# Kernel optimization log

Measured on AMD Instinct MI355X. Metric: run time of the kernel, lower is better.

Reference implementation:

```python
import jax, jax.numpy as jnp
import numpy as np

N_NODES = 50000
N_EDGES = 800000
D_IN = 64
D_HID = 64
N_LAYERS = 3
BN_EPS = 1e-5


def setup_inputs() -> dict:
    key = jax.random.key(0)
    ks = jax.random.split(key, 10)
    x = jax.random.normal(ks[0], (N_NODES, D_IN), dtype=jnp.float32)
    edge_index = jax.random.randint(ks[1], (2, N_EDGES), 0, N_NODES, dtype=jnp.int32)
    # Per-layer GCN weights (in==hid==64 so we can stack) and BatchNorm params.
    Ws = jax.random.normal(ks[2], (N_LAYERS, D_HID, D_HID), dtype=jnp.float32) / np.sqrt(D_HID)
    bs = jnp.zeros((N_LAYERS, D_HID), dtype=jnp.float32)
    gammas = jnp.ones((N_LAYERS, D_HID), dtype=jnp.float32)
    betas = jnp.zeros((N_LAYERS, D_HID), dtype=jnp.float32)
    means = jax.random.normal(ks[3], (N_LAYERS, D_HID), dtype=jnp.float32) * 0.1
    variances = jax.random.uniform(ks[4], (N_LAYERS, D_HID), dtype=jnp.float32, minval=0.5, maxval=1.5)
    lin_w = jax.random.normal(ks[5], (D_HID, 1), dtype=jnp.float32) / np.sqrt(D_HID)
    lin_b = jnp.zeros((1,), dtype=jnp.float32)
    return {"x": x, "edge_index": edge_index, "Ws": Ws, "bs": bs,
            "gammas": gammas, "betas": betas, "means": means,
            "variances": variances, "lin_w": lin_w, "lin_b": lin_b}


def _gnn_forward(x, edge_index, Ws, bs, gammas, betas, means, variances, lin_w, lin_b):
    n = x.shape[0]
    # GCNConv: add self loops, symmetric D^{-1/2}(A+I)D^{-1/2} normalization.
    loop = jnp.arange(n, dtype=edge_index.dtype)
    row = jnp.concatenate([edge_index[0], loop])  # source nodes
    col = jnp.concatenate([edge_index[1], loop])  # target nodes
    deg = jax.ops.segment_sum(jnp.ones(row.shape[0], x.dtype), col, num_segments=n)
    dinv = jax.lax.rsqrt(jnp.maximum(deg, 1.0))  # deg >= 1 from self loops
    norm = (dinv[row] * dinv[col])[:, None]  # [E+N, 1]

    h = x
    for i in range(N_LAYERS):
        h = h @ Ws[i]  # transform first (PyG GCNConv order)
        h = jax.ops.segment_sum(h[row] * norm, col, num_segments=n) + bs[i]
        # BatchNorm1d (eval mode: running stats) + ReLU; dropout is identity in eval.
        h = (h - means[i]) * jax.lax.rsqrt(variances[i] + BN_EPS) * gammas[i] + betas[i]
        h = jax.nn.relu(h)
    out = h @ lin_w + lin_b  # [N, 1]
    return out[:, 0]


def reference(x, edge_index, Ws, bs, gammas, betas, means, variances, lin_w, lin_b):
    return _gnn_forward(x, edge_index, Ws, bs, gammas, betas, means, variances, lin_w, lin_b)
```

## Files before the change

kernel.cpp:

```cpp
#include <hip/hip_runtime.h>
#include <hip/hip_bf16.h>


#define BN_EPS 1e-5f
#define CAP 64
#define CHUNK 4096
#define SEGCAP 5120
#define NBINS_MAX 256

__global__ __launch_bounds__(256) void k_bin_pairs(const int* __restrict__ row,
                                                   const int* __restrict__ col,
                                                   int* __restrict__ gfill,
                                                   unsigned int* __restrict__ gpairs,
                                                   int e, int nbins) {
    __shared__ unsigned int pl[CHUNK];
    __shared__ int bcnt[NBINS_MAX];
    __shared__ int bbase[NBINS_MAX];
    int tid = threadIdx.x;
    int base = blockIdx.x * CHUNK;
    for (int b = tid; b < nbins; b += 256) bcnt[b] = 0;
    __syncthreads();
    int nloc = e - base; if (nloc > CHUNK) nloc = CHUNK;
    #pragma unroll
    for (int it = 0; it < CHUNK / 1024; ++it) {
        int le = (it * 256 + tid) * 4;
        if (le + 3 < nloc) {
            int i4 = (base >> 2) + it * 256 + tid;
            int4 r = ((const int4*)row)[i4];
            int4 c = ((const int4*)col)[i4];
            atomicAdd(&bcnt[c.x >> 8], 1); pl[le + 0] = (unsigned)r.x | ((unsigned)c.x << 16);
            atomicAdd(&bcnt[c.y >> 8], 1); pl[le + 1] = (unsigned)r.y | ((unsigned)c.y << 16);
            atomicAdd(&bcnt[c.z >> 8], 1); pl[le + 2] = (unsigned)r.z | ((unsigned)c.z << 16);
            atomicAdd(&bcnt[c.w >> 8], 1); pl[le + 3] = (unsigned)r.w | ((unsigned)c.w << 16);
        } else {
            for (int j = 0; j < 4; ++j) {
                if (le + j < nloc) {
                    int rr = row[base + le + j];
                    int cc = col[base + le + j];
                    atomicAdd(&bcnt[cc >> 8], 1);
                    pl[le + j] = (unsigned)rr | ((unsigned)cc << 16);
                }
            }
        }
    }
    __syncthreads();
    for (int b = tid; b < nbins; b += 256) {
        bbase[b] = atomicAdd(&gfill[b], bcnt[b]);
        bcnt[b] = 0;
    }
    __syncthreads();
    for (int i = tid; i < nloc; i += 256) {
        unsigned int p = pl[i];
        int bin = p >> 24;
        int off = atomicAdd(&bcnt[bin], 1);
        int pos = bbase[bin] + off;
        if (pos < SEGCAP) gpairs[(size_t)bin * SEGCAP + pos] = p;
    }
}

__global__ __launch_bounds__(256) void k_bucket_build(const unsigned int* __restrict__ gpairs,
                                                      const int* __restrict__ gfill,
                                                      int* __restrict__ cnt,
                                                      unsigned short* __restrict__ bucket,
                                                      int n) {
    __shared__ unsigned short lb[256 * CAP];
    __shared__ int lc[256];
    int tid = threadIdx.x;
    int bin = blockIdx.x;
    lc[tid] = 0;
    __syncthreads();
    int m = gfill[bin]; if (m > SEGCAP) m = SEGCAP;
    const unsigned int* seg = gpairs + (size_t)bin * SEGCAP;
    for (int i = tid; i < m; i += 256) {
        unsigned int p = seg[i];
        int src = p & 0xffff;
        int dl = (p >> 16) & 255;
        int pos = atomicAdd(&lc[dl], 1);
        if (pos < CAP) lb[dl * CAP + pos] = (unsigned short)src;
    }
    __syncthreads();
    int nodebase = bin << 8;
    const int4* lb4 = (const int4*)lb;
    int4* gb4 = (int4*)bucket;
    for (int i = tid; i < 256 * 8; i += 256) {
        int rrow = i >> 3;
        int gnode = nodebase + rrow;
        if (gnode < n) gb4[(size_t)gnode * 8 + (i & 7)] = lb4[i];
    }
    int gnode = nodebase + tid;
    if (gnode < n) cnt[gnode] = lc[tid];
}

__global__ __launch_bounds__(256) void k_prescale(const float* __restrict__ x,
                                                  const int* __restrict__ cnt,
                                                  float* __restrict__ t, int n16) {
    int i = blockIdx.x * blockDim.x + threadIdx.x;
    if (i < n16) {
        int node = i >> 4;
        float d = rsqrtf((float)(cnt[node] + 1));
        float4 v = ((const float4*)x)[i];
        v.x *= d; v.y *= d; v.z *= d; v.w *= d;
        ((float4*)t)[i] = v;
    }
}

template<int LAYER, bool FINAL>
__global__ __launch_bounds__(256, 4) void k_layer(const float* __restrict__ t,
                                                  const int* __restrict__ cnt,
                                                  const unsigned short* __restrict__ bucket,
                                                  const float* __restrict__ W,
                                                  const float* __restrict__ bias,
                                                  const float* __restrict__ gamma,
                                                  const float* __restrict__ beta,
                                                  const float* __restrict__ mean,
                                                  const float* __restrict__ var,
                                                  float* __restrict__ hout,
                                                  const float* __restrict__ lw,
                                                  const float* __restrict__ lb,
                                                  float* __restrict__ outp, int n) {
    int lane = threadIdx.x & 63;
    float wreg[64];
    #pragma unroll
    for (int k = 0; k < 64; ++k) wreg[k] = W[k * 64 + lane];
    float bn_b  = bias[lane];
    float bn_m  = mean[lane];
    float bn_s  = gamma[lane] * rsqrtf(var[lane] + BN_EPS);
    float bn_be = beta[lane];
    float lwv   = FINAL ? lw[lane] : 0.f;
    int g = lane >> 4;
    int fl = (lane & 15) << 2;
    int wave = (blockIdx.x * blockDim.x + threadIdx.x) >> 6;
    int nwaves = (gridDim.x * blockDim.x) >> 6;
    for (int node = wave; node < n; node += nwaves) {
        int c = cnt[node];
        int myidx = (int)bucket[node * CAP + lane];
        float4 acc = {0.f, 0.f, 0.f, 0.f};
        int sub = 0;
        for (; sub + 8 <= c; sub += 8) {
            int sA = __shfl(myidx, sub + g, 64);
            int sB = __shfl(myidx, sub + 4 + g, 64);
            float4 vA = *(const float4*)(t + (size_t)sA * 64 + fl);
            float4 vB = *(const float4*)(t + (size_t)sB * 64 + fl);
            acc.x += vA.x; acc.y += vA.y; acc.z += vA.z; acc.w += vA.w;
            acc.x += vB.x; acc.y += vB.y; acc.z += vB.z; acc.w += vB.w;
        }
        for (; sub < c; sub += 4) {
            int j = sub + g;
            int jj = (j < c) ? j : c - 1;
            int sA = __shfl(myidx, jj, 64);
            if (j < c) {
                float4 v = *(const float4*)(t + (size_t)sA * 64 + fl);
                acc.x += v.x; acc.y += v.y; acc.z += v.z; acc.w += v.w;
            }
        }
        acc.x += __shfl_down(acc.x, 32, 64); acc.y += __shfl_down(acc.y, 32, 64);
        acc.z += __shfl_down(acc.z, 32, 64); acc.w += __shfl_down(acc.w, 32, 64);
        acc.x += __shfl_down(acc.x, 16, 64); acc.y += __shfl_down(acc.y, 16, 64);
        acc.z += __shfl_down(acc.z, 16, 64); acc.w += __shfl_down(acc.w, 16, 64);
        if (lane < 16) {
            float4 self = *(const float4*)(t + (size_t)node * 64 + fl);
            acc.x += self.x; acc.y += self.y; acc.z += self.z; acc.w += self.w;
        }
        float y = 0.f;
        #pragma unroll
        for (int q = 0; q < 16; ++q) {
            float ax = __shfl(acc.x, q, 64);
            float ay = __shfl(acc.y, q, 64);
            float az = __shfl(acc.z, q, 64);
            float aw = __shfl(acc.w, q, 64);
            y = fmaf(ax, wreg[4 * q + 0], y);
            y = fmaf(ay, wreg[4 * q + 1], y);
            y = fmaf(az, wreg[4 * q + 2], y);
            y = fmaf(aw, wreg[4 * q + 3], y);
        }
        float di = rsqrtf((float)(c + 1));
        float z = fmaf(y, di, bn_b);
        float h = fmaxf(fmaf(z - bn_m, bn_s, bn_be), 0.f);
        if (FINAL) {
            float p = h * lwv;
            p += __shfl_down(p, 32, 64);
            p += __shfl_down(p, 16, 64);
            p += __shfl_down(p, 8, 64);
            p += __shfl_down(p, 4, 64);
            p += __shfl_down(p, 2, 64);
            p += __shfl_down(p, 1, 64);
            if (lane == 0) outp[node] = p + lb[0];
        } else {
            hout[(size_t)node * 64 + lane] = h * di;
        }
    }
}

extern "C" void kernel_launch(void* const* d_in, const int* in_sizes, int n_in,
                              void* d_out, int out_size, void* d_ws, size_t ws_size,
                              hipStream_t stream) {
    const float* x    = (const float*)d_in[0];
    const int*   ei   = (const int*)d_in[1];
    const float* Ws   = (const float*)d_in[2];
    const float* bs   = (const float*)d_in[3];
    const float* gam  = (const float*)d_in[4];
    const float* bet  = (const float*)d_in[5];
    const float* mean = (const float*)d_in[6];
    const float* var  = (const float*)d_in[7];
    const float* lw   = (const float*)d_in[8];
    const float* lb   = (const float*)d_in[9];
    float* out = (float*)d_out;

    const int n = in_sizes[0] / 64;
    const int e = in_sizes[1] / 2;
    const int* row = ei;
    const int* col = ei + e;
    const int nbins = (n + 255) >> 8;

    int*   ws_i = (int*)d_ws;
    float* ws_f = (float*)d_ws;
    int* cnt = ws_i;
    int* gfill = ws_i + n;
    unsigned short* bucket = (unsigned short*)(ws_i + n + 256);
    float* tbuf = ws_f + n + 256 + 32 * (size_t)n;
    float* hbuf = tbuf + 64 * (size_t)n;
    unsigned int* gpairs = (unsigned int*)tbuf;

    int nb_p1 = (e + CHUNK - 1) / CHUNK;
    int n16 = n * 16;
    int nb_ps = (n16 + 255) / 256;
    int nb_ly = 1024;

    hipMemsetAsync(gfill, 0, 256 * sizeof(int), stream);
    k_bin_pairs<<<nb_p1, 256, 0, stream>>>(row, col, gfill, gpairs, e, nbins);
    k_bucket_build<<<nbins, 256, 0, stream>>>(gpairs, gfill, cnt, bucket, n);
    k_prescale<<<nb_ps, 256, 0, stream>>>(x, cnt, tbuf, n16);

    k_layer<0, false><<<nb_ly, 256, 0, stream>>>(tbuf, cnt, bucket, Ws,
                                                 bs, gam, bet, mean, var,
                                                 hbuf, nullptr, nullptr, nullptr, n);
    k_layer<1, false><<<nb_ly, 256, 0, stream>>>(hbuf, cnt, bucket, Ws + 4096,
                                                 bs + 64, gam + 64, bet + 64, mean + 64, var + 64,
                                                 tbuf, nullptr, nullptr, nullptr, n);
    k_layer<2, true><<<nb_ly, 256, 0, stream>>>(tbuf, cnt, bucket, Ws + 8192,
                                                bs + 128, gam + 128, bet + 128, mean + 128, var + 128,
                                                nullptr, lw, lb, out, n);
}
```

Before: 264.3 us.

## Store gathered node features in fp16 and regroup the per-node gather

The prescaled input and intermediate hidden features are now stored as fp16, which halves the bytes read in the random neighbor gathers of each layer. The gather is regrouped so that 8 lanes each load 8 halves per neighbor, covering 8 neighbors per load across the wave. Tail iterations use masking instead of a separate remainder loop. Occupancy hints and the grid size are also raised. Accumulation stays in fp32, but fp16 storage adds rounding error to the activations across the three layers.

```diff
diff --git a/kernel.cpp b/kernel.cpp
--- a/kernel.cpp
+++ b/kernel.cpp
@@ -1,5 +1,6 @@
 #include <hip/hip_runtime.h>
 #include <hip/hip_bf16.h>
+#include <hip/hip_fp16.h>
 
 
 #define BN_EPS 1e-5f
@@ -93,19 +94,24 @@
 
 __global__ __launch_bounds__(256) void k_prescale(const float* __restrict__ x,
                                                   const int* __restrict__ cnt,
-                                                  float* __restrict__ t, int n16) {
+                                                  __half* __restrict__ t, int n8) {
     int i = blockIdx.x * blockDim.x + threadIdx.x;
-    if (i < n16) {
-        int node = i >> 4;
+    if (i < n8) {
+        int node = i >> 3;
         float d = rsqrtf((float)(cnt[node] + 1));
-        float4 v = ((const float4*)x)[i];
-        v.x *= d; v.y *= d; v.z *= d; v.w *= d;
-        ((float4*)t)[i] = v;
+        const float4* xp = (const float4*)(x + (size_t)i * 8);
+        float4 a = xp[0], b = xp[1];
+        union { __half2 h2[4]; uint4 u; } o;
+        o.h2[0] = __floats2half2_rn(a.x * d, a.y * d);
+        o.h2[1] = __floats2half2_rn(a.z * d, a.w * d);
+        o.h2[2] = __floats2half2_rn(b.x * d, b.y * d);
+        o.h2[3] = __floats2half2_rn(b.z * d, b.w * d);
+        *(uint4*)(t + (size_t)i * 8) = o.u;
     }
 }
 
 template<int LAYER, bool FINAL>
-__global__ __launch_bounds__(256, 4) void k_layer(const float* __restrict__ t,
+__global__ __launch_bounds__(256, 6) void k_layer(const __half* __restrict__ t,
                                                   const int* __restrict__ cnt,
                                                   const unsigned short* __restrict__ bucket,
                                                   const float* __restrict__ W,
@@ -114,7 +120,7 @@
                                                   const float* __restrict__ beta,
                                                   const float* __restrict__ mean,
                                                   const float* __restrict__ var,
-                                                  float* __restrict__ hout,
+                                                  __half* __restrict__ hout,
                                                   const float* __restrict__ lw,
                                                   const float* __restrict__ lb,
                                                   float* __restrict__ outp, int n) {
@@ -127,52 +133,66 @@
     float bn_s  = gamma[lane] * rsqrtf(var[lane] + BN_EPS);
     float bn_be = beta[lane];
     float lwv   = FINAL ? lw[lane] : 0.f;
-    int g = lane >> 4;
-    int fl = (lane & 15) << 2;
+    int g = lane >> 3;
+    int q = lane & 7;
+    int qo = q << 3;
     int wave = (blockIdx.x * blockDim.x + threadIdx.x) >> 6;
     int nwaves = (gridDim.x * blockDim.x) >> 6;
+    union HV { float4 f4; __half2 h2[4]; };
     for (int node = wave; node < n; node += nwaves) {
         int c = cnt[node];
         int myidx = (int)bucket[node * CAP + lane];
-        float4 acc = {0.f, 0.f, 0.f, 0.f};
-        int sub = 0;
-        for (; sub + 8 <= c; sub += 8) {
-            int sA = __shfl(myidx, sub + g, 64);
-            int sB = __shfl(myidx, sub + 4 + g, 64);
-            float4 vA = *(const float4*)(t + (size_t)sA * 64 + fl);
-            float4 vB = *(const float4*)(t + (size_t)sB * 64 + fl);
-            acc.x += vA.x; acc.y += vA.y; acc.z += vA.z; acc.w += vA.w;
-            acc.x += vB.x; acc.y += vB.y; acc.z += vB.z; acc.w += vB.w;
-        }
-        for (; sub < c; sub += 4) {
-            int j = sub + g;
-            int jj = (j < c) ? j : c - 1;
-            int sA = __shfl(myidx, jj, 64);
-            if (j < c) {
-                float4 v = *(const float4*)(t + (size_t)sA * 64 + fl);
-                acc.x += v.x; acc.y += v.y; acc.z += v.z; acc.w += v.w;
-            }
-        }
-        acc.x += __shfl_down(acc.x, 32, 64); acc.y += __shfl_down(acc.y, 32, 64);
-        acc.z += __shfl_down(acc.z, 32, 64); acc.w += __shfl_down(acc.w, 32, 64);
-        acc.x += __shfl_down(acc.x, 16, 64); acc.y += __shfl_down(acc.y, 16, 64);
-        acc.z += __shfl_down(acc.z, 16, 64); acc.w += __shfl_down(acc.w, 16, 64);
-        if (lane < 16) {
-            float4 self = *(const float4*)(t + (size_t)node * 64 + fl);
-            acc.x += self.x; acc.y += self.y; acc.z += self.z; acc.w += self.w;
-        }
-        float y = 0.f;
+        float acc[8] = {0.f, 0.f, 0.f, 0.f, 0.f, 0.f, 0.f, 0.f};
+        for (int sub = 0; sub < c; sub += 16) {
+            int j1 = sub + g;
+            int j2 = sub + 8 + g;
+            int cm1 = c - 1;
+            int i1 = __shfl(myidx, (j1 < cm1 ? j1 : cm1), 64);
+            int i2 = __shfl(myidx, (j2 < cm1 ? j2 : cm1), 64);
+            float m1 = (j1 < c) ? 1.f : 0.f;
+            float m2 = (j2 < c) ? 1.f : 0.f;
+            HV v1, v2;
+            v1.f4 = *(const float4*)(t + ((size_t)i1 << 6) + qo);
+            v2.f4 = *(const float4*)(t + ((size_t)i2 << 6) + qo);
+            #pragma unroll
+            for (int p = 0; p < 4; ++p) {
+                float2 a = __half22float2(v1.h2[p]);
+                float2 b = __half22float2(v2.h2[p]);
+                acc[2 * p]     = fmaf(m1, a.x, acc[2 * p]);
+                acc[2 * p + 1] = fmaf(m1, a.y, acc[2 * p + 1]);
+                acc[2 * p]     = fmaf(m2, b.x, acc[2 * p]);
+                acc[2 * p + 1] = fmaf(m2, b.y, acc[2 * p + 1]);
+            }
+        }
+        {
+            float ms = (g == 0) ? 1.f : 0.f;
+            HV vs;
+            vs.f4 = *(const float4*)(t + ((size_t)node << 6) + qo);
+            #pragma unroll
+            for (int p = 0; p < 4; ++p) {
+                float2 a = __half22float2(vs.h2[p]);
+                acc[2 * p]     = fmaf(ms, a.x, acc[2 * p]);
+                acc[2 * p + 1] = fmaf(ms, a.y, acc[2 * p + 1]);
+            }
+        }
         #pragma unroll
-        for (int q = 0; q < 16; ++q) {
-            float ax = __shfl(acc.x, q, 64);
-            float ay = __shfl(acc.y, q, 64);
-            float az = __shfl(acc.z, q, 64);
-            float aw = __shfl(acc.w, q, 64);
-            y = fmaf(ax, wreg[4 * q + 0], y);
-            y = fmaf(ay, wreg[4 * q + 1], y);
-            y = fmaf(az, wreg[4 * q + 2], y);
-            y = fmaf(aw, wreg[4 * q + 3], y);
-        }
+        for (int i = 0; i < 8; ++i) {
+            acc[i] += __shfl_down(acc[i], 32, 64);
+            acc[i] += __shfl_down(acc[i], 16, 64);
+            acc[i] += __shfl_down(acc[i], 8, 64);
+        }
+        float y0 = 0.f, y1 = 0.f;
+        #pragma unroll
+        for (int q2 = 0; q2 < 8; ++q2) {
+            #pragma unroll
+            for (int i = 0; i < 8; i += 2) {
+                float a0 = __shfl(acc[i], q2, 64);
+                float a1 = __shfl(acc[i + 1], q2, 64);
+                y0 = fmaf(a0, wreg[8 * q2 + i], y0);
+                y1 = fmaf(a1, wreg[8 * q2 + i + 1], y1);
+            }
+        }
+        float y = y0 + y1;
         float di = rsqrtf((float)(c + 1));
         float z = fmaf(y, di, bn_b);
         float h = fmaxf(fmaf(z - bn_m, bn_s, bn_be), 0.f);
@@ -186,7 +206,7 @@
             p += __shfl_down(p, 1, 64);
             if (lane == 0) outp[node] = p + lb[0];
         } else {
-            hout[(size_t)node * 64 + lane] = h * di;
+            hout[(size_t)node * 64 + lane] = __float2half_rn(h * di);
         }
     }
 }
@@ -212,32 +232,31 @@
     const int* col = ei + e;
     const int nbins = (n + 255) >> 8;
 
-    int*   ws_i = (int*)d_ws;
-    float* ws_f = (float*)d_ws;
+    int* ws_i = (int*)d_ws;
     int* cnt = ws_i;
     int* gfill = ws_i + n;
     unsigned short* bucket = (unsigned short*)(ws_i + n + 256);
-    float* tbuf = ws_f + n + 256 + 32 * (size_t)n;
-    float* hbuf = tbuf + 64 * (size_t)n;
-    unsigned int* gpairs = (unsigned int*)tbuf;
+    __half* t16 = (__half*)(ws_i + n + 256 + 32 * (size_t)n);
+    __half* h16 = t16 + 64 * (size_t)n;
+    unsigned int* gpairs = (unsigned int*)t16;
 
     int nb_p1 = (e + CHUNK - 1) / CHUNK;
-    int n16 = n * 16;
-    int nb_ps = (n16 + 255) / 256;
-    int nb_ly = 1024;
+    int n8 = n * 8;
+    int nb_ps = (n8 + 255) / 256;
+    int nb_ly = 1536;
 
     hipMemsetAsync(gfill, 0, 256 * sizeof(int), stream);
     k_bin_pairs<<<nb_p1, 256, 0, stream>>>(row, col, gfill, gpairs, e, nbins);
     k_bucket_build<<<nbins, 256, 0, stream>>>(gpairs, gfill, cnt, bucket, n);
-    k_prescale<<<nb_ps, 256, 0, stream>>>(x, cnt, tbuf, n16);
-
-    k_layer<0, false><<<nb_ly, 256, 0, stream>>>(tbuf, cnt, bucket, Ws,
+    k_prescale<<<nb_ps, 256, 0, stream>>>(x, cnt, t16, n8);
+
+    k_layer<0, false><<<nb_ly, 256, 0, stream>>>(t16, cnt, bucket, Ws,
                                                  bs, gam, bet, mean, var,
-                                                 hbuf, nullptr, nullptr, nullptr, n);
-    k_layer<1, false><<<nb_ly, 256, 0, stream>>>(hbuf, cnt, bucket, Ws + 4096,
+                                                 h16, nullptr, nullptr, nullptr, n);
+    k_layer<1, false><<<nb_ly, 256, 0, stream>>>(h16, cnt, bucket, Ws + 4096,
                                                  bs + 64, gam + 64, bet + 64, mean + 64, var + 64,
-                                                 tbuf, nullptr, nullptr, nullptr, n);
-    k_layer<2, true><<<nb_ly, 256, 0, stream>>>(tbuf, cnt, bucket, Ws + 8192,
+                                                 t16, nullptr, nullptr, nullptr, n);
+    k_layer<2, true><<<nb_ly, 256, 0, stream>>>(t16, cnt, bucket, Ws + 8192,
                                                 bs + 128, gam + 128, bet + 128, mean + 128, var + 128,
                                                 nullptr, lw, lb, out, n);
 }
```

New measurement: 481.9 us. 1.82x slower.
